# Kernel optimization log

Hardware: AMD Instinct MI355X
Metric: run time of the kernel (lower is better)

Reference implementation:

```python
import jax, jax.numpy as jnp
import numpy as np

L, B, T, C, H, V = 4, 4, 1024, 1024, 16, 32000
DH = C // H
FF = 4 * C
IGNORE = 5
EPS = 1e-5


def setup_inputs() -> dict:
    key = jax.random.key(0)
    ks = jax.random.split(key, 12)
    s = 0.02
    return {
        "idx": jax.random.randint(ks[0], (B, T), 0, V),
        "targets": jax.random.randint(ks[1], (B, T), 0, V),
        "tok_emb": jax.random.normal(ks[2], (V, C), jnp.float32) * s,
        "pos_emb": jax.random.normal(ks[3], (T, C), jnp.float32) * s,
        "Wq": jax.random.normal(ks[4], (L, C, C), jnp.float32) * s,
        "Wk": jax.random.normal(ks[5], (L, C, C), jnp.float32) * s,
        "Wv": jax.random.normal(ks[6], (L, C, C), jnp.float32) * s,
        "Wo": jax.random.normal(ks[7], (L, C, C), jnp.float32) * s,
        "bo": jnp.zeros((L, C), jnp.float32),
        "ln1_g": jnp.ones((L, C), jnp.float32),
        "ln1_b": jnp.zeros((L, C), jnp.float32),
        "ln2_g": jnp.ones((L, C), jnp.float32),
        "ln2_b": jnp.zeros((L, C), jnp.float32),
        "W1": jax.random.normal(ks[8], (L, C, FF), jnp.float32) * s,
        "b1": jnp.zeros((L, FF), jnp.float32),
        "W2": jax.random.normal(ks[9], (L, FF, C), jnp.float32) * s,
        "b2": jnp.zeros((L, C), jnp.float32),
        "lnf_g": jnp.ones((C,), jnp.float32),
        "lnf_b": jnp.zeros((C,), jnp.float32),
        "Whead": jax.random.normal(ks[10], (C, V), jnp.float32) * s,
        "bhead": jnp.zeros((V,), jnp.float32),
    }


def _layernorm(x, g, b):
    mu = jnp.mean(x, axis=-1, keepdims=True)
    var = jnp.var(x, axis=-1, keepdims=True)
    return (x - mu) * jax.lax.rsqrt(var + EPS) * g + b


def _gpt_forward(idx, targets, tok_emb, pos_emb, Wq, Wk, Wv, Wo, bo,
                 ln1_g, ln1_b, ln2_g, ln2_b, W1, b1, W2, b2,
                 lnf_g, lnf_b, Whead, bhead):
    x = tok_emb[idx] + pos_emb[None, :, :]  # [B,T,C]
    causal = jnp.tril(jnp.ones((T, T), bool))
    for i in range(L):
        h = _layernorm(x, ln1_g[i], ln1_b[i])
        q = (h @ Wq[i]).reshape(B, T, H, DH)
        k = (h @ Wk[i]).reshape(B, T, H, DH)
        v = (h @ Wv[i]).reshape(B, T, H, DH)
        wei = jnp.einsum("bqhd,bkhd->bhqk", q, k) * (DH ** -0.5)
        wei = jnp.where(causal[None, None], wei, -jnp.inf)
        wei = jax.nn.softmax(wei, axis=-1)
        att = jnp.einsum("bhqk,bkhd->bqhd", wei, v).reshape(B, T, C)
        x = x + att @ Wo[i] + bo[i]
        h = _layernorm(x, ln2_g[i], ln2_b[i])
        x = x + jax.nn.gelu(h @ W1[i] + b1[i], approximate=False) @ W2[i] + b2[i]
    x = _layernorm(x, lnf_g, lnf_b)
    logits = x @ Whead + bhead  # [B,T,V]
    # cross-entropy with ignore_index=5
    lg = logits.reshape(B * T, V)
    tg = targets.reshape(B * T)
    logp = jax.nn.log_softmax(lg, axis=-1)
    nll = -jnp.take_along_axis(logp, tg[:, None], axis=-1)[:, 0]
    valid = (tg != IGNORE).astype(lg.dtype)
    loss = jnp.sum(nll * valid) / jnp.maximum(jnp.sum(valid), 1.0)
    return logits, loss


def reference(idx, targets, tok_emb, pos_emb, Wq, Wk, Wv, Wo, bo,
              ln1_g, ln1_b, ln2_g, ln2_b, W1, b1, W2, b2,
              lnf_g, lnf_b, Whead, bhead):
    return _gpt_forward(idx, targets, tok_emb, pos_emb, Wq, Wk, Wv, Wo, bo,
                        ln1_g, ln1_b, ln2_g, ln2_b, W1, b1, W2, b2,
                        lnf_g, lnf_b, Whead, bhead)
```

## Files before the change

kernel.cpp:

```cpp
#include <hip/hip_runtime.h>
#include <cstdint>
#include <cstddef>

#define Lx 4
#define Bx 4
#define Tx 1024
#define Cx 1024
#define Hx 16
#define DHx 64
#define FFx 4096
#define Vx 32000
#define BTx 4096

typedef __attribute__((ext_vector_type(8))) __bf16 bf16x8;
typedef __attribute__((ext_vector_type(4))) float f32x4;
typedef __attribute__((ext_vector_type(8))) short short8;

__device__ __forceinline__ float bflo(unsigned u){ return __builtin_bit_cast(float, u << 16); }
__device__ __forceinline__ float bf2f(short s){ return bflo((unsigned)(unsigned short)s); }
__device__ __forceinline__ short f2bf(float f){
  unsigned u = __builtin_bit_cast(unsigned, f);
  u += 0x7fffu + ((u >> 16) & 1u);
  return (short)(u >> 16);
}

__device__ __forceinline__ void gload_lds16(const short* g, short* l){
  __builtin_amdgcn_global_load_lds(
      (const __attribute__((address_space(1))) unsigned int*)g,
      (__attribute__((address_space(3))) unsigned int*)l, 16, 0, 0);
}

__device__ __forceinline__ int xcd_swizzle(int orig, int nwg){
  const int q = nwg >> 3, r = nwg & 7;
  const int xcd = orig & 7, wg = orig >> 3;
  const int base = (xcd < r) ? xcd * (q + 1) : r * (q + 1) + (xcd - r) * q;
  return base + wg;
}

__global__ __launch_bounds__(256) void embed_kernel(
    const int* __restrict__ idx, const float* __restrict__ tok,
    const float* __restrict__ pos, float* __restrict__ x)
{
  const int bt = blockIdx.x;
  const int t  = bt & (Tx - 1);
  const int tid = threadIdx.x;
  const int tk = idx[bt];
  float4 a = *(const float4*)&tok[((size_t)tk << 10) + (tid << 2)];
  const float4 p = *(const float4*)&pos[((size_t)t << 10) + (tid << 2)];
  a.x += p.x; a.y += p.y; a.z += p.z; a.w += p.w;
  *(float4*)&x[((size_t)bt << 10) + (tid << 2)] = a;
}

__global__ __launch_bounds__(256) void ln_kernel(
    const float* __restrict__ x, const float* __restrict__ g,
    const float* __restrict__ b, short* __restrict__ out)
{
  const int row = blockIdx.x;
  const int tid = threadIdx.x;
  const float4 v = *(const float4*)&x[((size_t)row << 10) + (tid << 2)];
  float s  = v.x + v.y + v.z + v.w;
  float ss = v.x*v.x + v.y*v.y + v.z*v.z + v.w*v.w;
  #pragma unroll
  for (int off = 32; off >= 1; off >>= 1) {
    s  += __shfl_down(s, off);
    ss += __shfl_down(ss, off);
  }
  __shared__ float rs[4], rss[4];
  const int lane = tid & 63, w = tid >> 6;
  if (lane == 0) { rs[w] = s; rss[w] = ss; }
  __syncthreads();
  s  = rs[0] + rs[1] + rs[2] + rs[3];
  ss = rss[0] + rss[1] + rss[2] + rss[3];
  const float mu  = s * (1.0f / Cx);
  const float var = ss * (1.0f / Cx) - mu * mu;
  const float rstd = rsqrtf(var + 1e-5f);
  const float4 g4 = *(const float4*)&g[tid << 2];
  const float4 b4 = *(const float4*)&b[tid << 2];
  short4 o;
  o.x = f2bf((v.x - mu) * rstd * g4.x + b4.x);
  o.y = f2bf((v.y - mu) * rstd * g4.y + b4.y);
  o.z = f2bf((v.z - mu) * rstd * g4.z + b4.z);
  o.w = f2bf((v.w - mu) * rstd * g4.w + b4.w);
  *(short4*)&out[((size_t)row << 10) + (tid << 2)] = o;
}

__global__ __launch_bounds__(256) void wconv_kernel(
    const float* __restrict__ W, short* __restrict__ Wt, int K, int N)
{
  __shared__ float tile[32][33];
  const int n0 = blockIdx.x << 5, k0 = blockIdx.y << 5;
  const int tx = threadIdx.x & 31, ty = threadIdx.x >> 5;
  #pragma unroll
  for (int r = 0; r < 4; ++r)
    tile[ty + (r << 3)][tx] = __builtin_nontemporal_load(
        &W[(size_t)(k0 + ty + (r << 3)) * N + n0 + tx]);
  __syncthreads();
  #pragma unroll
  for (int r = 0; r < 4; ++r)
    Wt[(size_t)(n0 + ty + (r << 3)) * K + k0 + tx] = f2bf(tile[tx][ty + (r << 3)]);
}

__global__ __launch_bounds__(256) void wconv4_kernel(
    const float* __restrict__ Wq, const float* __restrict__ Wk,
    const float* __restrict__ Wv, const float* __restrict__ Wo,
    short* __restrict__ qkvT, short* __restrict__ woT)
{
  __shared__ float tile[32][33];
  const int z = blockIdx.z;
  const float* W = (z == 0) ? Wq : (z == 1) ? Wk : (z == 2) ? Wv : Wo;
  short* Wt = (z < 3) ? qkvT + (size_t)z * Cx * Cx : woT;
  const int n0 = blockIdx.x << 5, k0 = blockIdx.y << 5;
  const int tx = threadIdx.x & 31, ty = threadIdx.x >> 5;
  #pragma unroll
  for (int r = 0; r < 4; ++r)
    tile[ty + (r << 3)][tx] = __builtin_nontemporal_load(
        &W[(size_t)(k0 + ty + (r << 3)) * Cx + n0 + tx]);
  __syncthreads();
  #pragma unroll
  for (int r = 0; r < 4; ++r)
    Wt[(size_t)(n0 + ty + (r << 3)) * Cx + k0 + tx] = f2bf(tile[tx][ty + (r << 3)]);
}

template<int MODE>
__global__ __launch_bounds__(256) void gemm_kernel(
    const short* __restrict__ A, const short* __restrict__ Bt,
    const float* __restrict__ bias, const float* __restrict__ res,
    float* __restrict__ outF, short* __restrict__ outB, int N, int K)
{
  __shared__ __align__(16) short sA[128 * 32];
  __shared__ __align__(16) short sB[128 * 32];
  const int tid  = threadIdx.x;
  const int lane = tid & 63;
  const int wave = tid >> 6;
  const int bid  = xcd_swizzle((int)blockIdx.x, (int)gridDim.x);
  const int tm = (bid & 31) << 7;
  const int tn = (bid >> 5) << 7;
  const int wm = ((wave >> 1) & 1) << 6;
  const int wn = (wave & 1) << 6;

  f32x4 acc[4][4] = {};

  const int o1  = tid << 4;
  const int row = o1 >> 6;
  const int col = (o1 & 63) >> 1;
  const short* gA1 = A  + (size_t)(tm + row) * K + col;
  const short* gA2 = A  + (size_t)(tm + row + 64) * K + col;
  const short* gB1 = Bt + (size_t)(tn + row) * K + col;
  const short* gB2 = Bt + (size_t)(tn + row + 64) * K + col;
  short* lA1 = sA + (wave << 9);
  short* lA2 = sA + 2048 + (wave << 9);
  short* lB1 = sB + (wave << 9);
  short* lB2 = sB + 2048 + (wave << 9);

  for (int k0 = 0; k0 < K; k0 += 32) {
    gload_lds16(gA1 + k0, lA1);
    gload_lds16(gA2 + k0, lA2);
    gload_lds16(gB1 + k0, lB1);
    gload_lds16(gB2 + k0, lB2);
    __syncthreads();
    bf16x8 aF[4], bF[4];
    const int kb = (lane >> 4) << 3;
    const int rsel = lane & 15;
    #pragma unroll
    for (int m = 0; m < 4; ++m)
      aF[m] = *(const bf16x8*)&sA[(wm + m * 16 + rsel) * 32 + kb];
    #pragma unroll
    for (int n = 0; n < 4; ++n)
      bF[n] = *(const bf16x8*)&sB[(wn + n * 16 + rsel) * 32 + kb];
    #pragma unroll
    for (int m = 0; m < 4; ++m) {
      #pragma unroll
      for (int n = 0; n < 4; ++n)
        acc[m][n] = __builtin_amdgcn_mfma_f32_16x16x32_bf16(aF[m], bF[n], acc[m][n], 0, 0, 0);
    }
    __syncthreads();
  }

  const int r0 = (lane >> 4) << 2;
  const int c0 = lane & 15;
  #pragma unroll
  for (int m = 0; m < 4; ++m) {
    #pragma unroll
    for (int n = 0; n < 4; ++n) {
      #pragma unroll
      for (int r = 0; r < 4; ++r) {
        const int grow = tm + wm + m * 16 + r0 + r;
        const int gcol = tn + wn + n * 16 + c0;
        const float v = acc[m][n][r];
        if constexpr (MODE == 0) {
          const int which = gcol >> 10;
          const int cc = gcol & 1023;
          const int b = grow >> 10, t = grow & 1023;
          const int hh = cc >> 6, d = cc & 63;
          outB[(size_t)which * (BTx * Cx) +
               ((size_t)((((b << 4) + hh) << 10) + t) << 6) + d] = f2bf(v);
        } else {
          const size_t o = (size_t)grow * N + gcol;
          outF[o] = res[o] + v + bias[gcol];
        }
      }
    }
  }
}

#define GBAR() do { __builtin_amdgcn_sched_barrier(0); __builtin_amdgcn_s_barrier(); __builtin_amdgcn_sched_barrier(0); } while(0)
#define VM4 asm volatile("s_waitcnt vmcnt(4)" ::: "memory");
#define VM0 asm volatile("s_waitcnt vmcnt(0)" ::: "memory");
#define NOWAIT

#define PHASE(qq, dd, STAGES, ENDW) do { \
  aF[0][0] = RD_A(dd, qq, 0, 0); aF[0][1] = RD_A(dd, qq, 0, 1); \
  aF[1][0] = RD_A(dd, qq, 1, 0); aF[1][1] = RD_A(dd, qq, 1, 1); \
  STAGES \
  GBAR(); \
  asm volatile("s_waitcnt lgkmcnt(0)" ::: "memory"); \
  __builtin_amdgcn_sched_barrier(0); \
  __builtin_amdgcn_s_setprio(1); \
  _Pragma("unroll") \
  for (int ks = 0; ks < 2; ++ks) { \
    _Pragma("unroll") \
    for (int mf = 0; mf < 2; ++mf) { \
      _Pragma("unroll") \
      for (int nf = 0; nf < 4; ++nf) \
        acc[((qq) << 1) + mf][nf] = __builtin_amdgcn_mfma_f32_16x16x32_bf16( \
            aF[mf][ks], bF[nf][ks], acc[((qq) << 1) + mf][nf], 0, 0, 0); \
    } \
  } \
  __builtin_amdgcn_s_setprio(0); \
  ENDW \
  GBAR(); \
} while (0)

#define BLOAD(dd) do { \
  _Pragma("unroll") \
  for (int nf = 0; nf < 4; ++nf) { bF[nf][0] = RD_B(dd, nf, 0); bF[nf][1] = RD_B(dd, nf, 1); } \
} while (0)

#define FINISH(qq) do { \
  _Pragma("unroll") \
  for (int m8 = ((qq) << 1); m8 < ((qq) << 1) + 2; ++m8) { \
    _Pragma("unroll") \
    for (int nf = 0; nf < 4; ++nf) { \
      _Pragma("unroll") \
      for (int r = 0; r < 4; ++r) { \
        const int grow = tm + (wm << 7) + (m8 << 4) + (g4 << 2) + r; \
        const int gcol = tn + (wn << 6) + (nf << 4) + r15; \
        if constexpr (MODE == 3) { \
          acc[m8][nf][r] += bb4[nf]; \
          outF[(size_t)grow * N + gcol] = acc[m8][nf][r]; \
        } else { \
          const float t2 = acc[m8][nf][r] + bb4[nf]; \
          const float gl = 0.5f * t2 * (1.0f + erff(t2 * 0.7071067811865475f)); \
          outB[(size_t)grow * N + gcol] = f2bf(gl); \
        } \
      } \
    } \
  } \
} while (0)

template<int MODE>
__global__ __launch_bounds__(512, 2) void gemm256_kernel(
    const short* __restrict__ A, const short* __restrict__ Bt,
    const float* __restrict__ bias, float* __restrict__ outF,
    short* __restrict__ outB, float* __restrict__ cep, int N, int K)
{
  __shared__ __align__(16) char lds[131072];
  const int tid  = threadIdx.x;
  const int lane = tid & 63;
  const int wid  = tid >> 6;
  const int wm   = wid >> 2;
  const int wn   = wid & 3;
  const int r15  = lane & 15;
  const int g4   = lane >> 4;
  const int bid  = xcd_swizzle((int)blockIdx.x, (int)gridDim.x);
  const int tm   = (bid & 15) << 8;
  const int tn   = (bid >> 4) << 8;
  const int NT   = K >> 6;
  const int NI   = NT >> 1;

  const int row0   = tid >> 3;
  const int innerE = ((tid & 7) ^ ((tid >> 3) & 7)) << 3;
  const int X0     = tid << 4;
  const short* srcA = A  + (size_t)(tm + row0) * K + innerE;
  const short* srcB = Bt + (size_t)(tn + row0) * K + innerE;
  const size_t h128K = (size_t)128 * K;
  const size_t r64K  = (size_t)64 * K;

  auto STAGE_A = [&](int t, int hh) {
    const short* s = srcA + (size_t)hh * h128K + (t << 6);
    char* d = lds + ((t & 1) << 15) + (hh << 14) + X0;
    gload_lds16(s, (short*)d);
    gload_lds16(s + r64K, (short*)(d + 8192));
  };
  auto STAGE_B = [&](int t, int hh) {
    const short* s = srcB + (size_t)hh * h128K + (t << 6);
    char* d = lds + 65536 + ((t & 1) << 15) + (hh << 14) + X0;
    gload_lds16(s, (short*)d);
    gload_lds16(s + r64K, (short*)(d + 8192));
  };

  const int arowb = (wm << 7) + r15;
  const int bcolb = (wn << 6) + r15;
  const int kchnk = g4 << 4;
  auto RD_A = [&](int d, int q, int mf, int ks) -> bf16x8 {
    const int row = arowb + (q << 5) + (mf << 4);
    return *(const bf16x8*)(lds + (d << 15) + (row << 7) +
                            ((((ks) << 6) + kchnk) ^ ((row & 7) << 4)));
  };
  auto RD_B = [&](int d, int nf, int ks) -> bf16x8 {
    const int colc = bcolb + (nf << 4);
    return *(const bf16x8*)(lds + 65536 + (d << 15) + (colc << 7) +
                            ((((ks) << 6) + kchnk) ^ ((colc & 7) << 4)));
  };

  f32x4 acc[8][4] = {};

  STAGE_A(0, 0); STAGE_A(0, 1); STAGE_B(0, 0); STAGE_B(0, 1);
  STAGE_B(1, 0); STAGE_B(1, 1);
  VM4
  GBAR();

  for (int i = 0; i < NI - 1; ++i) {
    const int t1 = 2 * i + 1;
    const int ta = 2 * i + 2;
    const int tb = 2 * i + 3;
    bf16x8 aF[2][2], bF[4][2];
    BLOAD(0);
    PHASE(0, 0, { STAGE_A(t1, 0); },                  NOWAIT);
    PHASE(1, 0, { STAGE_A(t1, 1); STAGE_B(ta, 0); },  NOWAIT);
    PHASE(2, 0, { STAGE_B(ta, 1); },                  NOWAIT);
    PHASE(3, 0, { },                                  VM4);
    BLOAD(1);
    PHASE(0, 1, { STAGE_A(ta, 0); },                  NOWAIT);
    PHASE(1, 1, { STAGE_A(ta, 1); STAGE_B(tb, 0); },  NOWAIT);
    PHASE(2, 1, { STAGE_B(tb, 1); },                  NOWAIT);
    PHASE(3, 1, { },                                  VM4);
  }

  float bb4[4];
  #pragma unroll
  for (int nf = 0; nf < 4; ++nf) bb4[nf] = bias[tn + (wn << 6) + (nf << 4) + r15];

  {
    bf16x8 aF[2][2], bF[4][2];
    BLOAD(0);
    PHASE(0, 0, { STAGE_A(NT - 1, 0); }, NOWAIT);
    PHASE(1, 0, { STAGE_A(NT - 1, 1); }, NOWAIT);
    PHASE(2, 0, { },                     NOWAIT);
    PHASE(3, 0, { },                     VM0);
    BLOAD(1);
    PHASE(0, 1, { }, NOWAIT); FINISH(0);
    PHASE(1, 1, { }, NOWAIT); FINISH(1);
    PHASE(2, 1, { }, NOWAIT); FINISH(2);
    PHASE(3, 1, { }, NOWAIT); FINISH(3);
  }

  if constexpr (MODE == 3) {
    const int nb = tn >> 8;
    float* cepart = (float*)lds;
    #pragma unroll
    for (int m8 = 0; m8 < 8; ++m8) {
      #pragma unroll
      for (int r = 0; r < 4; ++r) {
        float sm = __expf(acc[m8][0][r]) + __expf(acc[m8][1][r])
                 + __expf(acc[m8][2][r]) + __expf(acc[m8][3][r]);
        sm += __shfl_xor(sm, 1);
        sm += __shfl_xor(sm, 2);
        sm += __shfl_xor(sm, 4);
        sm += __shfl_xor(sm, 8);
        if (r15 == 0)
          cepart[(wn << 8) + (wm << 7) + (m8 << 4) + (g4 << 2) + r] = sm;
      }
    }
    __syncthreads();
    if (tid < 256) {
      const float S = cepart[tid] + cepart[256 + tid] + cepart[512 + tid] + cepart[768 + tid];
      cep[(size_t)(tm + tid) * 125 + nb] = S;
    }
  }
}

__global__ __launch_bounds__(512) void fattn_kernel(
    const short* __restrict__ q, const short* __restrict__ k,
    const short* __restrict__ v, short* __restrict__ att)
{
  __shared__ __align__(16) short sQ[8192];
  __shared__ __align__(16) short sK[2][4096];
  __shared__ __align__(16) short sVT[2][4096];
  __shared__ __align__(16) short sP[8][1024];

  const int tid  = threadIdx.x;
  const int lane = tid & 63;
  const int w    = tid >> 6;
  const int r15  = lane & 15;
  const int g4   = lane >> 4;
  const int bid  = xcd_swizzle((int)blockIdx.x, (int)gridDim.x);
  const int qb   = bid & 7;
  const int bh   = bid >> 3;

  const char* Qb = (const char*)(q + ((size_t)bh << 16)) + ((size_t)qb << 14);
  const char* Kb = (const char*)(k + ((size_t)bh << 16));
  const char* Vb = (const char*)(v + ((size_t)bh << 16));

  const int X0  = tid << 4;
  const int sw0 = X0 ^ (((X0 >> 7) & 7) << 4);
  const int X1  = X0 + 8192;
  const int sw1 = X1 ^ (((X1 >> 7) & 7) << 4);
  const int ldsW = (w << 10);

  const int vdh  = tid & 63;
  const int vkv0 = (tid >> 6) << 3;
  const int vb0  = (vdh * 128 + vkv0 * 2) ^ ((vdh & 7) << 4);

  auto stageK = [&](int kt, int buf) {
    const char* Kt = Kb + ((size_t)kt << 13);
    gload_lds16((const short*)(Kt + sw0), (short*)((char*)sK[buf] + ldsW));
  };
  auto loadV = [&](int kt, unsigned short* uv) {
    const char* Vt = Vb + ((size_t)kt << 13);
    #pragma unroll
    for (int j = 0; j < 8; ++j)
      uv[j] = *(const unsigned short*)(Vt + ((vkv0 + j) << 7) + (vdh << 1));
  };
  auto writeV = [&](int buf, const unsigned short* uv) {
    short8 p;
    #pragma unroll
    for (int j = 0; j < 8; ++j) p[j] = (short)uv[j];
    *(short8*)((char*)sVT[buf] + vb0) = p;
  };

  gload_lds16((const short*)(Qb + sw0), (short*)((char*)sQ + ldsW));
  gload_lds16((const short*)(Qb + sw1), (short*)((char*)sQ + ldsW + 8192));
  stageK(0, 0);
  {
    unsigned short uv[8];
    loadV(0, uv);
    writeV(0, uv);
  }
  __syncthreads();

  bf16x8 aQ[2];
  {
    const int qrow = (w << 4) + r15;
    const int base = qrow * 128 + (g4 << 4);
    const int sz = (qrow & 7) << 4;
    aQ[0] = *(const bf16x8*)((char*)sQ + ((base     ) ^ sz));
    aQ[1] = *(const bf16x8*)((char*)sQ + ((base + 64) ^ sz));
  }

  float m[4] = {-3e38f, -3e38f, -3e38f, -3e38f};
  float l[4] = {0.f, 0.f, 0.f, 0.f};
  f32x4 acc_o[4] = {};
  const int qrow_g0 = (qb << 7) + (w << 4) + (g4 << 2);
  const int ktmax = 2 * qb + 1;

  for (int kt = 0; kt <= ktmax; ++kt) {
    const int cur = kt & 1;
    unsigned short uv2[8];
    if (kt < ktmax) {
      stageK(kt + 1, cur ^ 1);
      loadV(kt + 1, uv2);
    }

    f32x4 s[4] = {};
    #pragma unroll
    for (int f = 0; f < 4; ++f) {
      const int kv = (f << 4) + r15;
      const int kb = kv * 128 + (g4 << 4);
      const int sz = (kv & 7) << 4;
      const bf16x8 b0 = *(const bf16x8*)((char*)sK[cur] + ((kb     ) ^ sz));
      const bf16x8 b1 = *(const bf16x8*)((char*)sK[cur] + ((kb + 64) ^ sz));
      s[f] = __builtin_amdgcn_mfma_f32_16x16x32_bf16(aQ[0], b0, s[f], 0, 0, 0);
      s[f] = __builtin_amdgcn_mfma_f32_16x16x32_bf16(aQ[1], b1, s[f], 0, 0, 0);
    }
    #pragma unroll
    for (int f = 0; f < 4; ++f) {
      #pragma unroll
      for (int r = 0; r < 4; ++r) {
        float sv = s[f][r] * 0.125f;
        if ((kt << 6) + (f << 4) + r15 > qrow_g0 + r) sv = -3e38f;
        s[f][r] = sv;
      }
    }
    #pragma unroll
    for (int r = 0; r < 4; ++r) {
      float mx = fmaxf(fmaxf(s[0][r], s[1][r]), fmaxf(s[2][r], s[3][r]));
      mx = fmaxf(mx, __shfl_xor(mx, 1));
      mx = fmaxf(mx, __shfl_xor(mx, 2));
      mx = fmaxf(mx, __shfl_xor(mx, 4));
      mx = fmaxf(mx, __shfl_xor(mx, 8));
      const float mn = fmaxf(m[r], mx);
      const float e  = __expf(m[r] - mn);
      float sum = 0.f;
      #pragma unroll
      for (int f = 0; f < 4; ++f) {
        const float p = __expf(s[f][r] - mn);
        s[f][r] = p; sum += p;
      }
      sum += __shfl_xor(sum, 1);
      sum += __shfl_xor(sum, 2);
      sum += __shfl_xor(sum, 4);
      sum += __shfl_xor(sum, 8);
      l[r] = l[r] * e + sum;
      m[r] = mn;
      acc_o[0][r] *= e; acc_o[1][r] *= e; acc_o[2][r] *= e; acc_o[3][r] *= e;
    }
    short* Pw = sP[w];
    #pragma unroll
    for (int f = 0; f < 4; ++f) {
      #pragma unroll
      for (int r = 0; r < 4; ++r) {
        const int prow = (g4 << 2) + r;
        const int byte = prow * 128 + (((f << 4) + r15) << 1);
        *(short*)((char*)Pw + (byte ^ ((prow & 7) << 4))) = f2bf(s[f][r]);
      }
    }
    #pragma unroll
    for (int ks = 0; ks < 2; ++ks) {
      const int ab = r15 * 128 + (ks << 6) + (g4 << 4);
      const bf16x8 aP = *(const bf16x8*)((char*)Pw + (ab ^ ((r15 & 7) << 4)));
      #pragma unroll
      for (int f = 0; f < 4; ++f) {
        const int dh = (f << 4) + r15;
        const int bb = dh * 128 + (ks << 6) + (g4 << 4);
        const bf16x8 bV = *(const bf16x8*)((char*)sVT[cur] + (bb ^ ((dh & 7) << 4)));
        acc_o[f] = __builtin_amdgcn_mfma_f32_16x16x32_bf16(aP, bV, acc_o[f], 0, 0, 0);
      }
    }

    if (kt < ktmax) writeV(cur ^ 1, uv2);
    __syncthreads();
  }

  const int b = bh >> 4, hh = bh & 15;
  #pragma unroll
  for (int f = 0; f < 4; ++f) {
    #pragma unroll
    for (int r = 0; r < 4; ++r) {
      const int qg = qrow_g0 + r;
      const int dh = (f << 4) + r15;
      att[((size_t)((b << 10) + qg) << 10) + (hh << 6) + dh] = f2bf(acc_o[f][r] / l[r]);
    }
  }
}

__global__ __launch_bounds__(256) void ce_lse_kernel(
    const float* __restrict__ part, const float* __restrict__ logits,
    const int* __restrict__ tgt, float2* __restrict__ nll)
{
  const int row  = blockIdx.x * 4 + (threadIdx.x >> 6);
  const int lane = threadIdx.x & 63;
  float S = 0.f;
  #pragma unroll
  for (int p = 0; p < 2; ++p) {
    const int i = lane + (p << 6);
    if (i < 125) S += part[(size_t)row * 125 + i];
  }
  #pragma unroll
  for (int off = 32; off >= 1; off >>= 1) S += __shfl_xor(S, off);
  if (lane == 0) {
    const int tg = tgt[row];
    float v = 0.f, cnt = 0.f;
    if (tg != 5) {
      const float lt = logits[(size_t)row * Vx + tg];
      v = -(lt - logf(S));
      cnt = 1.f;
    }
    float2 o2; o2.x = v; o2.y = cnt;
    nll[row] = o2;
  }
}

__global__ __launch_bounds__(256) void ce_sum_kernel(
    const float2* __restrict__ nll, float* __restrict__ out)
{
  const int tid = threadIdx.x;
  float s = 0.f, c = 0.f;
  #pragma unroll
  for (int i = 0; i < 16; ++i) {
    const float2 v = nll[tid * 16 + i];
    s += v.x; c += v.y;
  }
  __shared__ float ls[256], lc[256];
  ls[tid] = s; lc[tid] = c;
  __syncthreads();
  for (int off = 128; off >= 1; off >>= 1) {
    if (tid < off) { ls[tid] += ls[tid + off]; lc[tid] += lc[tid + off]; }
    __syncthreads();
  }
  if (tid == 0) out[131072000ull] = ls[0] / fmaxf(lc[0], 1.0f);
}

extern "C" void kernel_launch(void* const* d_in, const int* in_sizes, int n_in,
                              void* d_out, int out_size, void* d_ws, size_t ws_size,
                              hipStream_t stream)
{
  const int*   idx     = (const int*)d_in[0];
  const int*   targets = (const int*)d_in[1];
  const float* tok_emb = (const float*)d_in[2];
  const float* pos_emb = (const float*)d_in[3];
  const float* Wq      = (const float*)d_in[4];
  const float* Wk      = (const float*)d_in[5];
  const float* Wv      = (const float*)d_in[6];
  const float* Wo      = (const float*)d_in[7];
  const float* bo      = (const float*)d_in[8];
  const float* ln1_g   = (const float*)d_in[9];
  const float* ln1_b   = (const float*)d_in[10];
  const float* ln2_g   = (const float*)d_in[11];
  const float* ln2_b   = (const float*)d_in[12];
  const float* W1      = (const float*)d_in[13];
  const float* b1      = (const float*)d_in[14];
  const float* W2      = (const float*)d_in[15];
  const float* b2      = (const float*)d_in[16];
  const float* lnf_g   = (const float*)d_in[17];
  const float* lnf_b   = (const float*)d_in[18];
  const float* Whead   = (const float*)d_in[19];
  const float* bhead   = (const float*)d_in[20];
  float* out = (float*)d_out;

  char* ws = (char*)d_ws;
  size_t off = 0;
  auto alloc = [&](size_t bytes) -> char* {
    char* p = ws + off;
    off += (bytes + 255) & ~(size_t)255;
    return p;
  };
  float* x    = (float*)alloc((size_t)BTx * Cx * 4);
  short* h    = (short*)alloc((size_t)BTx * Cx * 2);
  char*  blk  = ws + off;
  short* qb   = (short*)alloc((size_t)BTx * Cx * 2);
  short* kb   = (short*)alloc((size_t)BTx * Cx * 2);
  short* vb   = (short*)alloc((size_t)BTx * Cx * 2);
  short* attb = (short*)alloc((size_t)BTx * Cx * 2);
  short* ffb  = (short*)alloc((size_t)BTx * FFx * 2);
  short* wheadT = (short*)blk;
  short* wqkvT = (short*)alloc((size_t)3 * Cx * Cx * 2);
  short* woT  = (short*)alloc((size_t)Cx * Cx * 2);
  short* w1T  = (short*)alloc((size_t)Cx * FFx * 2);
  short* w2T  = (short*)alloc((size_t)FFx * Cx * 2);
  if (ws_size < off) return;
  float* part  = (float*)wqkvT;
  float2* nllb = (float2*)woT;

  embed_kernel<<<BTx, 256, 0, stream>>>(idx, tok_emb, pos_emb, x);

  for (int i = 0; i < Lx; ++i) {
    const size_t wo_off = (size_t)i * Cx * Cx;
    const size_t w1_off = (size_t)i * Cx * FFx;
    wconv4_kernel<<<dim3(Cx / 32, Cx / 32, 4), 256, 0, stream>>>(
        Wq + wo_off, Wk + wo_off, Wv + wo_off, Wo + wo_off, wqkvT, woT);
    wconv_kernel<<<dim3(FFx / 32, Cx / 32), 256, 0, stream>>>(W1 + w1_off, w1T, Cx, FFx);
    wconv_kernel<<<dim3(Cx / 32, FFx / 32), 256, 0, stream>>>(W2 + w1_off, w2T, FFx, Cx);

    ln_kernel<<<BTx, 256, 0, stream>>>(x, ln1_g + i * Cx, ln1_b + i * Cx, h);
    gemm_kernel<0><<<32 * 24, 256, 0, stream>>>(h, wqkvT, nullptr, nullptr, nullptr, qb, 3 * Cx, Cx);
    fattn_kernel<<<Bx * Hx * (Tx / 128), 512, 0, stream>>>(qb, kb, vb, attb);
    gemm_kernel<1><<<32 * 8, 256, 0, stream>>>(attb, woT, bo + i * Cx, x, x, nullptr, Cx, Cx);

    ln_kernel<<<BTx, 256, 0, stream>>>(x, ln2_g + i * Cx, ln2_b + i * Cx, h);
    gemm256_kernel<2><<<16 * 16, 512, 0, stream>>>(h, w1T, b1 + i * FFx, nullptr, ffb, nullptr, FFx, Cx);
    gemm_kernel<1><<<32 * 8, 256, 0, stream>>>(ffb, w2T, b2 + i * Cx, x, x, nullptr, Cx, FFx);
  }

  ln_kernel<<<BTx, 256, 0, stream>>>(x, lnf_g, lnf_b, h);
  wconv_kernel<<<dim3(Vx / 32, Cx / 32), 256, 0, stream>>>(Whead, wheadT, Cx, Vx);
  gemm256_kernel<3><<<16 * 125, 512, 0, stream>>>(h, wheadT, bhead, out, nullptr, part, Vx, Cx);

  ce_lse_kernel<<<BTx / 4, 256, 0, stream>>>(part, out, targets, nllb);
  ce_sum_kernel<<<1, 256, 0, stream>>>(nllb, out);
}
```

Before: 1.621 ms.

## Shrink flash-attention query tile to 64 rows with 256-thread blocks

The attention kernel now handles 64 query rows per block with 4 waves instead of 128 rows with 8 waves, doubling the grid to 1024 blocks. K tiles are staged with two async loads per thread, and V transposition loads 32-bit pairs so each thread writes two transposed rows. The goal is finer causal work granularity, less diagonal waste and better load balance and occupancy, at the cost of re-reading K/V from global memory twice as often per head.

```diff
diff --git a/kernel.cpp b/kernel.cpp
--- a/kernel.cpp
+++ b/kernel.cpp
@@ -380,14 +380,14 @@
   }
 }
 
-__global__ __launch_bounds__(512) void fattn_kernel(
+__global__ __launch_bounds__(256) void fattn_kernel(
     const short* __restrict__ q, const short* __restrict__ k,
     const short* __restrict__ v, short* __restrict__ att)
 {
-  __shared__ __align__(16) short sQ[8192];
+  __shared__ __align__(16) short sQ[4096];
   __shared__ __align__(16) short sK[2][4096];
   __shared__ __align__(16) short sVT[2][4096];
-  __shared__ __align__(16) short sP[8][1024];
+  __shared__ __align__(16) short sP[4][1024];
 
   const int tid  = threadIdx.x;
   const int lane = tid & 63;
@@ -395,45 +395,52 @@
   const int r15  = lane & 15;
   const int g4   = lane >> 4;
   const int bid  = xcd_swizzle((int)blockIdx.x, (int)gridDim.x);
-  const int qb   = bid & 7;
-  const int bh   = bid >> 3;
-
-  const char* Qb = (const char*)(q + ((size_t)bh << 16)) + ((size_t)qb << 14);
+  const int qt   = bid & 15;
+  const int bh   = bid >> 4;
+
+  const char* Qb = (const char*)(q + ((size_t)bh << 16)) + ((size_t)qt << 13);
   const char* Kb = (const char*)(k + ((size_t)bh << 16));
   const char* Vb = (const char*)(v + ((size_t)bh << 16));
 
   const int X0  = tid << 4;
+  const int X1  = X0 + 4096;
   const int sw0 = X0 ^ (((X0 >> 7) & 7) << 4);
-  const int X1  = X0 + 8192;
   const int sw1 = X1 ^ (((X1 >> 7) & 7) << 4);
-  const int ldsW = (w << 10);
-
-  const int vdh  = tid & 63;
-  const int vkv0 = (tid >> 6) << 3;
-  const int vb0  = (vdh * 128 + vkv0 * 2) ^ ((vdh & 7) << 4);
-
+  const int ldsOff0 = (w << 10);
+  const int ldsOff1 = (w << 10) + 4096;
+
+  const int vdh  = (lane & 31) << 1;
+  const int vkv0 = (((w << 1) + (lane >> 5)) << 3);
+  const int vb0  = (vdh * 128 + vkv0 * 2)       ^ ((vdh & 7) << 4);
+  const int vb1  = ((vdh + 1) * 128 + vkv0 * 2) ^ (((vdh + 1) & 7) << 4);
+
+  auto loadV = [&](int kt, unsigned* uv) {
+    const char* Vt = Vb + ((size_t)kt << 13);
+    #pragma unroll
+    for (int j = 0; j < 8; ++j)
+      uv[j] = *(const unsigned*)(Vt + ((vkv0 + j) << 7) + (vdh << 1));
+  };
+  auto writeV = [&](int buf, const unsigned* uv) {
+    short8 plo, phi;
+    #pragma unroll
+    for (int j = 0; j < 8; ++j) {
+      plo[j] = (short)(uv[j] & 0xffffu);
+      phi[j] = (short)(uv[j] >> 16);
+    }
+    *(short8*)((char*)sVT[buf] + vb0) = plo;
+    *(short8*)((char*)sVT[buf] + vb1) = phi;
+  };
   auto stageK = [&](int kt, int buf) {
     const char* Kt = Kb + ((size_t)kt << 13);
-    gload_lds16((const short*)(Kt + sw0), (short*)((char*)sK[buf] + ldsW));
-  };
-  auto loadV = [&](int kt, unsigned short* uv) {
-    const char* Vt = Vb + ((size_t)kt << 13);
-    #pragma unroll
-    for (int j = 0; j < 8; ++j)
-      uv[j] = *(const unsigned short*)(Vt + ((vkv0 + j) << 7) + (vdh << 1));
-  };
-  auto writeV = [&](int buf, const unsigned short* uv) {
-    short8 p;
-    #pragma unroll
-    for (int j = 0; j < 8; ++j) p[j] = (short)uv[j];
-    *(short8*)((char*)sVT[buf] + vb0) = p;
-  };
-
-  gload_lds16((const short*)(Qb + sw0), (short*)((char*)sQ + ldsW));
-  gload_lds16((const short*)(Qb + sw1), (short*)((char*)sQ + ldsW + 8192));
+    gload_lds16((const short*)(Kt + sw0), (short*)((char*)sK[buf] + ldsOff0));
+    gload_lds16((const short*)(Kt + sw1), (short*)((char*)sK[buf] + ldsOff1));
+  };
+
+  gload_lds16((const short*)(Qb + sw0), (short*)((char*)sQ + ldsOff0));
+  gload_lds16((const short*)(Qb + sw1), (short*)((char*)sQ + ldsOff1));
   stageK(0, 0);
   {
-    unsigned short uv[8];
+    unsigned uv[8];
     loadV(0, uv);
     writeV(0, uv);
   }
@@ -451,13 +458,12 @@
   float m[4] = {-3e38f, -3e38f, -3e38f, -3e38f};
   float l[4] = {0.f, 0.f, 0.f, 0.f};
   f32x4 acc_o[4] = {};
-  const int qrow_g0 = (qb << 7) + (w << 4) + (g4 << 2);
-  const int ktmax = 2 * qb + 1;
-
-  for (int kt = 0; kt <= ktmax; ++kt) {
+  const int qrow_g0 = (qt << 6) + (w << 4) + (g4 << 2);
+
+  for (int kt = 0; kt <= qt; ++kt) {
     const int cur = kt & 1;
-    unsigned short uv2[8];
-    if (kt < ktmax) {
+    unsigned uv2[8];
+    if (kt < qt) {
       stageK(kt + 1, cur ^ 1);
       loadV(kt + 1, uv2);
     }
@@ -528,7 +534,7 @@
       }
     }
 
-    if (kt < ktmax) writeV(cur ^ 1, uv2);
+    if (kt < qt) writeV(cur ^ 1, uv2);
     __syncthreads();
   }
 
@@ -654,7 +660,7 @@
 
     ln_kernel<<<BTx, 256, 0, stream>>>(x, ln1_g + i * Cx, ln1_b + i * Cx, h);
     gemm_kernel<0><<<32 * 24, 256, 0, stream>>>(h, wqkvT, nullptr, nullptr, nullptr, qb, 3 * Cx, Cx);
-    fattn_kernel<<<Bx * Hx * (Tx / 128), 512, 0, stream>>>(qb, kb, vb, attb);
+    fattn_kernel<<<Bx * Hx * (Tx / 64), 256, 0, stream>>>(qb, kb, vb, attb);
     gemm_kernel<1><<<32 * 8, 256, 0, stream>>>(attb, woT, bo + i * Cx, x, x, nullptr, Cx, Cx);
 
     ln_kernel<<<BTx, 256, 0, stream>>>(x, ln2_g + i * Cx, ln2_b + i * Cx, h);
```

Measured after the change: 1.554 ms. -4.1%, faster.
